# Kernel tuning notes

Hardware: AMD Instinct MI355X
Metric: run time of the kernel (lower is better)

## Reference

```python
import jax, jax.numpy as jnp
import numpy as np

NOT_EPSILON = 1.0
B, Q, K, T = 2, 512, 512, 256  # batch, num queries, num keys, dims


def swishmax(x, axis):
    # x * exp(x - max) / (sum(|x * exp(x - max)|) + 1)
    xexp = x * jnp.exp(x - jnp.max(x, axis=axis, keepdims=True))
    return xexp / (jnp.sum(jnp.abs(xexp), axis=axis, keepdims=True) + NOT_EPSILON)


def setup_inputs() -> dict:
    key = jax.random.key(0)
    ks = jax.random.split(key, 8)
    s = 1.0 / np.sqrt(T)
    return {
        "query_tokens": jax.random.normal(ks[0], (B, Q, T), jnp.float32),
        "key_tokens": jax.random.normal(ks[1], (B, K, T), jnp.float32),
        "value_tokens": jax.random.normal(ks[2], (B, K, T), jnp.float32),
        "Wk": jax.random.normal(ks[3], (T, T), jnp.float32) * s,
        "Wq": jax.random.normal(ks[4], (T, T), jnp.float32) * s,
        "Wva": jax.random.normal(ks[5], (T, T), jnp.float32) * s,
        "Wal": jax.random.normal(ks[6], (T, T), jnp.float32) * s,
        "Wvo": jax.random.normal(ks[7], (T, T), jnp.float32) * s,
    }


def reference(query_tokens, key_tokens, value_tokens, Wk, Wq, Wva, Wal, Wvo):
    # torch nn.Linear: y = x @ W.T (no biases)
    k = jnp.einsum('bkt,ut->bku', key_tokens, Wk)      # [B,K,T]
    q = jnp.einsum('bqt,ut->bqu', query_tokens, Wq)    # [B,Q,T]
    # elementwise outer product over token pairs: [B,K,Q,T]
    raw = k[:, :, None, :] * q[:, None, :, :]
    logits = jnp.einsum('bkqt,ut->bkqu', raw, Wal)     # [B,K,Q,T]
    scale = swishmax(logits, axis=-2)                  # normalize over Q
    v = jnp.einsum('bkt,ut->bku', value_tokens, Wva)   # [B,K,T]
    values_scaled = v[:, :, None, :] * scale           # [B,K,Q,T]
    value_sum = values_scaled.sum(axis=-3)             # sum over K -> [B,Q,T]
    return jnp.einsum('bqt,ut->bqu', value_sum, Wvo)   # [B,Q,T]
```

## Files before the change

### kernel.cpp

```cpp
#include <hip/hip_runtime.h>
#include <cstdint>


typedef short bf16x8 __attribute__((ext_vector_type(8)));
typedef float f32x4  __attribute__((ext_vector_type(4)));

__device__ inline float bf2f(short s) {
  return __uint_as_float(((unsigned)(unsigned short)s) << 16);
}
__device__ inline unsigned packrn(float lo, float hi) {
  return __builtin_amdgcn_perm(__float_as_uint(hi) + 0x8000u,
                               __float_as_uint(lo) + 0x8000u, 0x07060302u);
}

#define FMA16()                                                                 \
  c[0][0] += a.x*w.x; c[0][1] += a.x*w.y; c[0][2] += a.x*w.z; c[0][3] += a.x*w.w; \
  c[1][0] += a.y*w.x; c[1][1] += a.y*w.y; c[1][2] += a.y*w.z; c[1][3] += a.y*w.w; \
  c[2][0] += a.z*w.x; c[2][1] += a.z*w.y; c[2][2] += a.z*w.z; c[2][3] += a.z*w.w; \
  c[3][0] += a.w*w.x; c[3][1] += a.w*w.y; c[3][2] += a.w*w.z; c[3][3] += a.w*w.w;

#define GEMM_BODY(X, WT)                                                        \
  __shared__ __align__(16) float As[16][68];                                    \
  __shared__ __align__(16) float Ws[16][64];                                    \
  const int tid = threadIdx.x;                                                  \
  const int tx4 = (tid & 15) * 4;                                               \
  const int ty4 = (tid >> 4) * 4;                                               \
  const int m0 = blockIdx.x * 64, u0 = blockIdx.y * 64;                         \
  const int lmi = tid >> 2, lc4 = (tid & 3) * 4;                                \
  const int lr  = tid >> 4, lu4 = (tid & 15) * 4;                               \
  float c[4][4] = {};                                                           \
  _Pragma("unroll 1")                                                           \
  for (int t0 = 0; t0 < 256; t0 += 16) {                                        \
    const float4 xa = *(const float4*)&(X)[(size_t)(m0 + lmi) * 256 + t0 + lc4];\
    const float4 wb = *(const float4*)&(WT)[(size_t)(t0 + lr) * 256 + u0 + lu4];\
    __syncthreads();                                                            \
    As[lc4 + 0][lmi] = xa.x; As[lc4 + 1][lmi] = xa.y;                           \
    As[lc4 + 2][lmi] = xa.z; As[lc4 + 3][lmi] = xa.w;                           \
    *(float4*)&Ws[lr][lu4] = wb;                                                \
    __syncthreads();                                                            \
    _Pragma("unroll")                                                           \
    for (int t = 0; t < 16; ++t) {                                              \
      const float4 a = *(const float4*)&As[t][ty4];                             \
      const float4 w = *(const float4*)&Ws[t][tx4];                             \
      FMA16();                                                                  \
    }                                                                           \
  }

__global__ __launch_bounds__(256) void prep(
    const float* __restrict__ Wk, const float* __restrict__ Wq,
    const float* __restrict__ Wva, const float* __restrict__ Wvo,
    const float* __restrict__ Wal, float* __restrict__ WT,
    short* __restrict__ WalF)
{
  const int r = blockIdx.x;
  const int m = blockIdx.y;
  const int t = threadIdx.x;
  if (m < 4) {
    const float* W = (m == 0) ? Wk : (m == 1) ? Wq : (m == 2) ? Wva : Wvo;
    WT[(size_t)m * 65536 + (size_t)t * 256 + r] = W[r * 256 + t];
  } else {
    const float v = Wal[r * 256 + t];
    const int uc = r >> 5, uu = r & 31, cc = t >> 3, j = t & 7;
    WalF[((size_t)(uc * 32 + cc) * 32 + uu) * 8 + j] = (short)packrn(v, v);
  }
}

__global__ __launch_bounds__(256) void proj3(
    const float* __restrict__ key, const float* __restrict__ value,
    const float* __restrict__ query, const float* __restrict__ WT,
    float* __restrict__ kproj, float* __restrict__ vproj, short* __restrict__ qpF)
{
  const int z = blockIdx.z;
  const float* X  = (z == 0) ? key : (z == 1) ? value : query;
  const float* Wt = WT + (size_t)((z == 0) ? 0 : (z == 1) ? 2 : 1) * 65536;
  GEMM_BODY(X, Wt);
  if (z == 2) {
    const int tbase = u0 + tx4;
    const int ks = tbase >> 5, l4f = (tbase & 31) >> 3, j0 = tbase & 7;
#pragma unroll
    for (int i = 0; i < 4; ++i) {
      const int m = m0 + ty4 + i;
      const int bb = m >> 9, q = m & 511;
      const int g = q >> 4, l15q = q & 15;
      const size_t idx = ((size_t)(((bb * 32 + g) * 8 + ks) * 64) + l4f * 16 + l15q) * 8 + j0;
      uint2 s; s.x = packrn(c[i][0], c[i][1]); s.y = packrn(c[i][2], c[i][3]);
      *(uint2*)&qpF[idx] = s;
    }
  } else {
    float* C = (z == 0) ? kproj : vproj;
#pragma unroll
    for (int i = 0; i < 4; ++i)
      *(float4*)&C[(size_t)(m0 + ty4 + i) * 256 + u0 + tx4] =
          make_float4(c[i][0], c[i][1], c[i][2], c[i][3]);
  }
}

__global__ __launch_bounds__(256) void gemm_out(
    const float* __restrict__ X, const float* __restrict__ WT, float* __restrict__ out)
{
  GEMM_BODY(X, WT);
#pragma unroll
  for (int i = 0; i < 4; ++i)
    *(float4*)&out[(size_t)(m0 + ty4 + i) * 256 + u0 + tx4] =
        make_float4(c[i][0], c[i][1], c[i][2], c[i][3]);
}

__global__ __launch_bounds__(1024, 4) void kernelC(
    const short* __restrict__ qpF, const float* __restrict__ kproj,
    const float* __restrict__ vproj, const short* __restrict__ WalF,
    float* __restrict__ vsum)
{
  __shared__ __align__(16) short W2F[8192];
  __shared__ float mS[16][32];
  __shared__ float sS[16][32];
  __shared__ float gS[32];

  const int kt = blockIdx.x, uc = blockIdx.y, b = blockIdx.z;
  const int u0 = uc * 32, k0 = kt * 32;
  const int tid = threadIdx.x;
  const int lane = tid & 63, w = tid >> 6;
  const int l15 = lane & 15, l4 = lane >> 4;
  const int c8 = tid >> 5;

  float wvf[8];
  {
    const bf16x8 wv = *(const bf16x8*)&WalF[((size_t)uc * 1024 + tid) * 8];
#pragma unroll
    for (int j = 0; j < 8; ++j) wvf[j] = bf2f(wv[j]);
  }

  const short* qbase = qpF + (size_t)b * 131072;
  const f32x4 z4 = {0.f, 0.f, 0.f, 0.f};
  f32x4 acc[2][2] = {z4, z4, z4, z4};

#pragma unroll 1
  for (int kk = 0; kk < 32; ++kk) {
    const int k = k0 + kk;
    const long krow = (long)(b * 512 + k) * 256;
    const f32x4 kp0 = *(const f32x4*)&kproj[krow + c8 * 8];
    const f32x4 kp1 = *(const f32x4*)&kproj[krow + c8 * 8 + 4];
    __syncthreads();
    {
      uint4 st;
      st.x = packrn(wvf[0] * kp0[0], wvf[1] * kp0[1]);
      st.y = packrn(wvf[2] * kp0[2], wvf[3] * kp0[3]);
      st.z = packrn(wvf[4] * kp1[0], wvf[5] * kp1[1]);
      st.w = packrn(wvf[6] * kp1[2], wvf[7] * kp1[3]);
      *(uint4*)&W2F[tid * 8] = st;
    }
    __syncthreads();

    f32x4 lg[2][2] = {z4, z4, z4, z4};
#pragma unroll
    for (int ks = 0; ks < 8; ++ks) {
      const bf16x8 qa0 = *(const bf16x8*)&qbase[(((w * 2 + 0) * 8 + ks) * 64 + lane) * 8];
      const bf16x8 qa1 = *(const bf16x8*)&qbase[(((w * 2 + 1) * 8 + ks) * 64 + lane) * 8];
      const bf16x8 wf0 = *(const bf16x8*)&W2F[(((ks * 4 + l4) * 32) + l15) * 8];
      const bf16x8 wf1 = *(const bf16x8*)&W2F[(((ks * 4 + l4) * 32) + 16 + l15) * 8];
      lg[0][0] = __builtin_amdgcn_mfma_f32_16x16x32_bf16(qa0, wf0, lg[0][0], 0, 0, 0);
      lg[1][0] = __builtin_amdgcn_mfma_f32_16x16x32_bf16(qa1, wf0, lg[1][0], 0, 0, 0);
      lg[0][1] = __builtin_amdgcn_mfma_f32_16x16x32_bf16(qa0, wf1, lg[0][1], 0, 0, 0);
      lg[1][1] = __builtin_amdgcn_mfma_f32_16x16x32_bf16(qa1, wf1, lg[1][1], 0, 0, 0);
    }

#pragma unroll
    for (int ug = 0; ug < 2; ++ug) {
      float m = lg[0][ug][0];
#pragma unroll
      for (int qg = 0; qg < 2; ++qg)
#pragma unroll
        for (int i = 0; i < 4; ++i) m = fmaxf(m, lg[qg][ug][i]);
      float s = 0.f;
#pragma unroll
      for (int qg = 0; qg < 2; ++qg)
#pragma unroll
        for (int i = 0; i < 4; ++i) {
          const float x = lg[qg][ug][i];
          const float p = x * __expf(x);
          lg[qg][ug][i] = p;
          s += fabsf(p);
        }
      m = fmaxf(m, __shfl_xor(m, 16));
      m = fmaxf(m, __shfl_xor(m, 32));
      s += __shfl_xor(s, 16);
      s += __shfl_xor(s, 32);
      if (l4 == 0) { mS[w][ug * 16 + l15] = m; sS[w][ug * 16 + l15] = s; }
    }
    __syncthreads();
    if (tid < 32) {
      float M = mS[0][tid], S = sS[0][tid];
#pragma unroll
      for (int r = 1; r < 16; ++r) { M = fmaxf(M, mS[r][tid]); S += sS[r][tid]; }
      const float em = __expf(-M);
      gS[tid] = vproj[krow + u0 + tid] * em / fmaf(S, em, 1.0f);
    }
    __syncthreads();
    const float g0 = gS[l15], g1 = gS[16 + l15];
#pragma unroll
    for (int qg = 0; qg < 2; ++qg)
#pragma unroll
      for (int i = 0; i < 4; ++i) {
        acc[qg][0][i] = fmaf(g0, lg[qg][0][i], acc[qg][0][i]);
        acc[qg][1][i] = fmaf(g1, lg[qg][1][i], acc[qg][1][i]);
      }
  }

#pragma unroll
  for (int qg = 0; qg < 2; ++qg)
#pragma unroll
    for (int ug = 0; ug < 2; ++ug)
#pragma unroll
      for (int i = 0; i < 4; ++i)
        atomicAdd(&vsum[(size_t)(b * 512 + w * 32 + qg * 16 + l4 * 4 + i) * 256 +
                        u0 + ug * 16 + l15],
                  acc[qg][ug][i]);
}

extern "C" void kernel_launch(void* const* d_in, const int* in_sizes, int n_in,
                              void* d_out, int out_size, void* d_ws, size_t ws_size,
                              hipStream_t stream) {
  const float* query = (const float*)d_in[0];
  const float* key   = (const float*)d_in[1];
  const float* value = (const float*)d_in[2];
  const float* Wk    = (const float*)d_in[3];
  const float* Wq    = (const float*)d_in[4];
  const float* Wva   = (const float*)d_in[5];
  const float* Wal   = (const float*)d_in[6];
  const float* Wvo   = (const float*)d_in[7];
  float* ws = (float*)d_ws;

  float* WT    = ws;
  float* kproj = ws + 262144;
  float* vproj = kproj + 262144;
  float* vsum  = vproj + 262144;
  short* qpF   = (short*)(vsum + 262144);
  short* WalF  = qpF + 262144;
  float* out   = (float*)d_out;

  hipMemsetAsync(vsum, 0, 262144 * sizeof(float), stream);

  prep<<<dim3(256, 5), 256, 0, stream>>>(Wk, Wq, Wva, Wvo, Wal, WT, WalF);
  proj3<<<dim3(16, 4, 3), 256, 0, stream>>>(key, value, query, WT, kproj, vproj, qpF);
  kernelC<<<dim3(16, 8, 2), 1024, 0, stream>>>(qpF, kproj, vproj, WalF, vsum);
  gemm_out<<<dim3(16, 4), 256, 0, stream>>>(vsum, WT + 3 * 65536, out);
}
```

Measured before the change: 211.6 us.

## Drop prep kernel and memset, register-cache query fragments, double-buffer W2F in kernelC

The transpose and prep kernel and the memset are removed. The GEMMs now read row-major weights directly, and the Wal reformat plus the vsum zeroing run as an extra z-slice of proj3, cutting the launch count from five to three. kernelC moves to 512 threads, with each wave keeping its 64 query rows of bf16 fragments resident in registers instead of reloading them every k. The per-k W2F tile is double-buffered, with the next k's kproj loaded ahead so one barrier per iteration is removed. Shared-memory atomics with a rotating triple buffer replace the two-stage max/sum reduction. This adds heavy register pressure (128 VGPRs of query fragments plus accumulators), which may hurt occupancy.

```diff
diff --git a/kernel.cpp b/kernel.cpp
--- a/kernel.cpp
+++ b/kernel.cpp
@@ -11,6 +11,14 @@
 __device__ inline unsigned packrn(float lo, float hi) {
   return __builtin_amdgcn_perm(__float_as_uint(hi) + 0x8000u,
                                __float_as_uint(lo) + 0x8000u, 0x07060302u);
+}
+__device__ inline unsigned encM(float f) {
+  unsigned k = (unsigned)__float_as_int(f);
+  return (k & 0x80000000u) ? ~k : (k | 0x80000000u);
+}
+__device__ inline float decM(unsigned k) {
+  int i = (k & 0x80000000u) ? (int)(k ^ 0x80000000u) : (int)~k;
+  return __int_as_float(i);
 }
 
 #define FMA16()                                                                 \
@@ -19,24 +27,24 @@
   c[2][0] += a.z*w.x; c[2][1] += a.z*w.y; c[2][2] += a.z*w.z; c[2][3] += a.z*w.w; \
   c[3][0] += a.w*w.x; c[3][1] += a.w*w.y; c[3][2] += a.w*w.z; c[3][3] += a.w*w.w;
 
-#define GEMM_BODY(X, WT)                                                        \
+#define GEMM_BODY_RM(X, W)                                                      \
   __shared__ __align__(16) float As[16][68];                                    \
-  __shared__ __align__(16) float Ws[16][64];                                    \
+  __shared__ __align__(16) float Ws[16][68];                                    \
   const int tid = threadIdx.x;                                                  \
   const int tx4 = (tid & 15) * 4;                                               \
   const int ty4 = (tid >> 4) * 4;                                               \
   const int m0 = blockIdx.x * 64, u0 = blockIdx.y * 64;                         \
   const int lmi = tid >> 2, lc4 = (tid & 3) * 4;                                \
-  const int lr  = tid >> 4, lu4 = (tid & 15) * 4;                               \
   float c[4][4] = {};                                                           \
   _Pragma("unroll 1")                                                           \
   for (int t0 = 0; t0 < 256; t0 += 16) {                                        \
     const float4 xa = *(const float4*)&(X)[(size_t)(m0 + lmi) * 256 + t0 + lc4];\
-    const float4 wb = *(const float4*)&(WT)[(size_t)(t0 + lr) * 256 + u0 + lu4];\
+    const float4 wb = *(const float4*)&(W)[(size_t)(u0 + lmi) * 256 + t0 + lc4];\
     __syncthreads();                                                            \
     As[lc4 + 0][lmi] = xa.x; As[lc4 + 1][lmi] = xa.y;                           \
     As[lc4 + 2][lmi] = xa.z; As[lc4 + 3][lmi] = xa.w;                           \
-    *(float4*)&Ws[lr][lu4] = wb;                                                \
+    Ws[lc4 + 0][lmi] = wb.x; Ws[lc4 + 1][lmi] = wb.y;                           \
+    Ws[lc4 + 2][lmi] = wb.z; Ws[lc4 + 3][lmi] = wb.w;                           \
     __syncthreads();                                                            \
     _Pragma("unroll")                                                           \
     for (int t = 0; t < 16; ++t) {                                              \
@@ -46,34 +54,34 @@
     }                                                                           \
   }
 
-__global__ __launch_bounds__(256) void prep(
-    const float* __restrict__ Wk, const float* __restrict__ Wq,
-    const float* __restrict__ Wva, const float* __restrict__ Wvo,
-    const float* __restrict__ Wal, float* __restrict__ WT,
-    short* __restrict__ WalF)
-{
-  const int r = blockIdx.x;
-  const int m = blockIdx.y;
-  const int t = threadIdx.x;
-  if (m < 4) {
-    const float* W = (m == 0) ? Wk : (m == 1) ? Wq : (m == 2) ? Wva : Wvo;
-    WT[(size_t)m * 65536 + (size_t)t * 256 + r] = W[r * 256 + t];
-  } else {
-    const float v = Wal[r * 256 + t];
-    const int uc = r >> 5, uu = r & 31, cc = t >> 3, j = t & 7;
-    WalF[((size_t)(uc * 32 + cc) * 32 + uu) * 8 + j] = (short)packrn(v, v);
-  }
-}
-
 __global__ __launch_bounds__(256) void proj3(
     const float* __restrict__ key, const float* __restrict__ value,
-    const float* __restrict__ query, const float* __restrict__ WT,
-    float* __restrict__ kproj, float* __restrict__ vproj, short* __restrict__ qpF)
+    const float* __restrict__ query, const float* __restrict__ Wk,
+    const float* __restrict__ Wq, const float* __restrict__ Wva,
+    const float* __restrict__ Wal, float* __restrict__ kproj,
+    float* __restrict__ vproj, short* __restrict__ qpF,
+    short* __restrict__ WalF, float* __restrict__ vsum)
 {
   const int z = blockIdx.z;
-  const float* X  = (z == 0) ? key : (z == 1) ? value : query;
-  const float* Wt = WT + (size_t)((z == 0) ? 0 : (z == 1) ? 2 : 1) * 65536;
-  GEMM_BODY(X, Wt);
+  if (z == 3) {
+    const int p = blockIdx.x * 4 + blockIdx.y;
+    const int t256 = threadIdx.x;
+#pragma unroll
+    for (int e = 0; e < 4; ++e) {
+      const int d = p * 1024 + t256 * 4 + e;
+      const int j = d & 7, uu = (d >> 3) & 31, c8g = d >> 8;
+      const int ucx = c8g >> 5, cc = c8g & 31;
+      const float v = Wal[(ucx * 32 + uu) * 256 + cc * 8 + j];
+      WalF[d] = (short)packrn(v, v);
+    }
+    float4* vz = (float4*)(vsum + p * 4096);
+#pragma unroll
+    for (int e = 0; e < 4; ++e) vz[t256 * 4 + e] = make_float4(0.f, 0.f, 0.f, 0.f);
+    return;
+  }
+  const float* X = (z == 0) ? key : (z == 1) ? value : query;
+  const float* W = (z == 0) ? Wk  : (z == 1) ? Wva   : Wq;
+  GEMM_BODY_RM(X, W);
   if (z == 2) {
     const int tbase = u0 + tx4;
     const int ks = tbase >> 5, l4f = (tbase & 31) >> 3, j0 = tbase & 7;
@@ -96,83 +104,133 @@
 }
 
 __global__ __launch_bounds__(256) void gemm_out(
-    const float* __restrict__ X, const float* __restrict__ WT, float* __restrict__ out)
+    const float* __restrict__ X, const float* __restrict__ W, float* __restrict__ out)
 {
-  GEMM_BODY(X, WT);
+  GEMM_BODY_RM(X, W);
 #pragma unroll
   for (int i = 0; i < 4; ++i)
     *(float4*)&out[(size_t)(m0 + ty4 + i) * 256 + u0 + tx4] =
         make_float4(c[i][0], c[i][1], c[i][2], c[i][3]);
 }
 
-__global__ __launch_bounds__(1024, 4) void kernelC(
+union Frag { bf16x8 v; unsigned u[4]; };
+
+__global__ __launch_bounds__(512, 2) void kernelC(
     const short* __restrict__ qpF, const float* __restrict__ kproj,
     const float* __restrict__ vproj, const short* __restrict__ WalF,
     float* __restrict__ vsum)
 {
-  __shared__ __align__(16) short W2F[8192];
-  __shared__ float mS[16][32];
-  __shared__ float sS[16][32];
-  __shared__ float gS[32];
+  __shared__ __align__(16) short W2F[2][8192];
+  __shared__ float vpS[32 * 33];
+  __shared__ unsigned statM[96];
+  __shared__ float statS[96];
 
   const int kt = blockIdx.x, uc = blockIdx.y, b = blockIdx.z;
   const int u0 = uc * 32, k0 = kt * 32;
   const int tid = threadIdx.x;
   const int lane = tid & 63, w = tid >> 6;
   const int l15 = lane & 15, l4 = lane >> 4;
-  const int c8 = tid >> 5;
-
-  float wvf[8];
+  const int uu = tid & 31, c8 = tid >> 5;
+
+  if (tid < 96) { statM[tid] = 0u; statS[tid] = 0.f; }
   {
-    const bf16x8 wv = *(const bf16x8*)&WalF[((size_t)uc * 1024 + tid) * 8];
-#pragma unroll
-    for (int j = 0; j < 8; ++j) wvf[j] = bf2f(wv[j]);
+    const int kk = tid >> 4, uu2 = (tid & 15) * 2;
+    const float2 v2 = *(const float2*)&vproj[(size_t)(b * 512 + k0 + kk) * 256 + u0 + uu2];
+    vpS[kk * 33 + uu2] = v2.x; vpS[kk * 33 + uu2 + 1] = v2.y;
+  }
+
+  float wl0[8], wl1[8];
+  {
+    const bf16x8 w0 = *(const bf16x8*)&WalF[((size_t)(uc * 32 + c8) * 32 + uu) * 8];
+    const bf16x8 w1 = *(const bf16x8*)&WalF[((size_t)(uc * 32 + c8 + 16) * 32 + uu) * 8];
+#pragma unroll
+    for (int j = 0; j < 8; ++j) { wl0[j] = bf2f(w0[j]); wl1[j] = bf2f(w1[j]); }
   }
 
   const short* qbase = qpF + (size_t)b * 131072;
+  Frag qa[4][8];
+#pragma unroll
+  for (int qg = 0; qg < 4; ++qg)
+#pragma unroll
+    for (int ks = 0; ks < 8; ++ks) {
+      qa[qg][ks].v = *(const bf16x8*)&qbase[(((size_t)(w * 4 + qg) * 8 + ks) * 64 + lane) * 8];
+      asm volatile("" : "+v"(qa[qg][ks].u[0]), "+v"(qa[qg][ks].u[1]),
+                        "+v"(qa[qg][ks].u[2]), "+v"(qa[qg][ks].u[3]));
+    }
+
+  {
+    const long krow = (long)(b * 512 + k0) * 256;
+    const f32x4 a0 = *(const f32x4*)&kproj[krow + c8 * 8];
+    const f32x4 a1 = *(const f32x4*)&kproj[krow + c8 * 8 + 4];
+    const f32x4 b0 = *(const f32x4*)&kproj[krow + (c8 + 16) * 8];
+    const f32x4 b1 = *(const f32x4*)&kproj[krow + (c8 + 16) * 8 + 4];
+    uint4 st;
+    st.x = packrn(wl0[0] * a0[0], wl0[1] * a0[1]);
+    st.y = packrn(wl0[2] * a0[2], wl0[3] * a0[3]);
+    st.z = packrn(wl0[4] * a1[0], wl0[5] * a1[1]);
+    st.w = packrn(wl0[6] * a1[2], wl0[7] * a1[3]);
+    *(uint4*)&W2F[0][(c8 * 32 + uu) * 8] = st;
+    st.x = packrn(wl1[0] * b0[0], wl1[1] * b0[1]);
+    st.y = packrn(wl1[2] * b0[2], wl1[3] * b0[3]);
+    st.z = packrn(wl1[4] * b1[0], wl1[5] * b1[1]);
+    st.w = packrn(wl1[6] * b1[2], wl1[7] * b1[3]);
+    *(uint4*)&W2F[0][((c8 + 16) * 32 + uu) * 8] = st;
+  }
+  __syncthreads();
+
   const f32x4 z4 = {0.f, 0.f, 0.f, 0.f};
-  f32x4 acc[2][2] = {z4, z4, z4, z4};
+  f32x4 acc[4][2] = {z4, z4, z4, z4, z4, z4, z4, z4};
 
 #pragma unroll 1
   for (int kk = 0; kk < 32; ++kk) {
-    const int k = k0 + kk;
-    const long krow = (long)(b * 512 + k) * 256;
-    const f32x4 kp0 = *(const f32x4*)&kproj[krow + c8 * 8];
-    const f32x4 kp1 = *(const f32x4*)&kproj[krow + c8 * 8 + 4];
-    __syncthreads();
-    {
+    const int cs = kk & 1, ss = kk % 3;
+
+    f32x4 a0, a1, b0, b1;
+    if (kk < 31) {
+      const long krn = (long)(b * 512 + k0 + kk + 1) * 256;
+      a0 = *(const f32x4*)&kproj[krn + c8 * 8];
+      a1 = *(const f32x4*)&kproj[krn + c8 * 8 + 4];
+      b0 = *(const f32x4*)&kproj[krn + (c8 + 16) * 8];
+      b1 = *(const f32x4*)&kproj[krn + (c8 + 16) * 8 + 4];
+    }
+
+    f32x4 lg[4][2] = {z4, z4, z4, z4, z4, z4, z4, z4};
+#pragma unroll
+    for (int ks = 0; ks < 8; ++ks) {
+      const bf16x8 f0 = *(const bf16x8*)&W2F[cs][((ks * 4 + l4) * 32 + l15) * 8];
+      const bf16x8 f1 = *(const bf16x8*)&W2F[cs][((ks * 4 + l4) * 32 + 16 + l15) * 8];
+#pragma unroll
+      for (int qg = 0; qg < 4; ++qg) {
+        lg[qg][0] = __builtin_amdgcn_mfma_f32_16x16x32_bf16(qa[qg][ks].v, f0, lg[qg][0], 0, 0, 0);
+        lg[qg][1] = __builtin_amdgcn_mfma_f32_16x16x32_bf16(qa[qg][ks].v, f1, lg[qg][1], 0, 0, 0);
+      }
+    }
+
+    if (kk < 31) {
       uint4 st;
-      st.x = packrn(wvf[0] * kp0[0], wvf[1] * kp0[1]);
-      st.y = packrn(wvf[2] * kp0[2], wvf[3] * kp0[3]);
-      st.z = packrn(wvf[4] * kp1[0], wvf[5] * kp1[1]);
-      st.w = packrn(wvf[6] * kp1[2], wvf[7] * kp1[3]);
-      *(uint4*)&W2F[tid * 8] = st;
-    }
-    __syncthreads();
-
-    f32x4 lg[2][2] = {z4, z4, z4, z4};
-#pragma unroll
-    for (int ks = 0; ks < 8; ++ks) {
-      const bf16x8 qa0 = *(const bf16x8*)&qbase[(((w * 2 + 0) * 8 + ks) * 64 + lane) * 8];
-      const bf16x8 qa1 = *(const bf16x8*)&qbase[(((w * 2 + 1) * 8 + ks) * 64 + lane) * 8];
-      const bf16x8 wf0 = *(const bf16x8*)&W2F[(((ks * 4 + l4) * 32) + l15) * 8];
-      const bf16x8 wf1 = *(const bf16x8*)&W2F[(((ks * 4 + l4) * 32) + 16 + l15) * 8];
-      lg[0][0] = __builtin_amdgcn_mfma_f32_16x16x32_bf16(qa0, wf0, lg[0][0], 0, 0, 0);
-      lg[1][0] = __builtin_amdgcn_mfma_f32_16x16x32_bf16(qa1, wf0, lg[1][0], 0, 0, 0);
-      lg[0][1] = __builtin_amdgcn_mfma_f32_16x16x32_bf16(qa0, wf1, lg[0][1], 0, 0, 0);
-      lg[1][1] = __builtin_amdgcn_mfma_f32_16x16x32_bf16(qa1, wf1, lg[1][1], 0, 0, 0);
-    }
-
+      st.x = packrn(wl0[0] * a0[0], wl0[1] * a0[1]);
+      st.y = packrn(wl0[2] * a0[2], wl0[3] * a0[3]);
+      st.z = packrn(wl0[4] * a1[0], wl0[5] * a1[1]);
+      st.w = packrn(wl0[6] * a1[2], wl0[7] * a1[3]);
+      *(uint4*)&W2F[cs ^ 1][(c8 * 32 + uu) * 8] = st;
+      st.x = packrn(wl1[0] * b0[0], wl1[1] * b0[1]);
+      st.y = packrn(wl1[2] * b0[2], wl1[3] * b0[3]);
+      st.z = packrn(wl1[4] * b1[0], wl1[5] * b1[1]);
+      st.w = packrn(wl1[6] * b1[2], wl1[7] * b1[3]);
+      *(uint4*)&W2F[cs ^ 1][((c8 + 16) * 32 + uu) * 8] = st;
+    }
+
+    float Mv[2], Sv[2];
 #pragma unroll
     for (int ug = 0; ug < 2; ++ug) {
       float m = lg[0][ug][0];
 #pragma unroll
-      for (int qg = 0; qg < 2; ++qg)
+      for (int qg = 0; qg < 4; ++qg)
 #pragma unroll
         for (int i = 0; i < 4; ++i) m = fmaxf(m, lg[qg][ug][i]);
       float s = 0.f;
 #pragma unroll
-      for (int qg = 0; qg < 2; ++qg)
+      for (int qg = 0; qg < 4; ++qg)
 #pragma unroll
         for (int i = 0; i < 4; ++i) {
           const float x = lg[qg][ug][i];
@@ -184,34 +242,40 @@
       m = fmaxf(m, __shfl_xor(m, 32));
       s += __shfl_xor(s, 16);
       s += __shfl_xor(s, 32);
-      if (l4 == 0) { mS[w][ug * 16 + l15] = m; sS[w][ug * 16 + l15] = s; }
+      Mv[ug] = m; Sv[ug] = s;
+    }
+    if (l4 == 0) {
+      atomicMax(&statM[ss * 32 + l15],      encM(Mv[0]));
+      atomicMax(&statM[ss * 32 + 16 + l15], encM(Mv[1]));
+      atomicAdd(&statS[ss * 32 + l15],      Sv[0]);
+      atomicAdd(&statS[ss * 32 + 16 + l15], Sv[1]);
     }
     __syncthreads();
-    if (tid < 32) {
-      float M = mS[0][tid], S = sS[0][tid];
-#pragma unroll
-      for (int r = 1; r < 16; ++r) { M = fmaxf(M, mS[r][tid]); S += sS[r][tid]; }
+
+#pragma unroll
+    for (int ug = 0; ug < 2; ++ug) {
+      const int ui = ug * 16 + l15;
+      const float M = decM(statM[ss * 32 + ui]);
+      const float S = statS[ss * 32 + ui];
       const float em = __expf(-M);
-      gS[tid] = vproj[krow + u0 + tid] * em / fmaf(S, em, 1.0f);
-    }
-    __syncthreads();
-    const float g0 = gS[l15], g1 = gS[16 + l15];
-#pragma unroll
-    for (int qg = 0; qg < 2; ++qg)
-#pragma unroll
-      for (int i = 0; i < 4; ++i) {
-        acc[qg][0][i] = fmaf(g0, lg[qg][0][i], acc[qg][0][i]);
-        acc[qg][1][i] = fmaf(g1, lg[qg][1][i], acc[qg][1][i]);
-      }
-  }
-
-#pragma unroll
-  for (int qg = 0; qg < 2; ++qg)
+      const float g = vpS[kk * 33 + ui] * em / fmaf(S, em, 1.0f);
+#pragma unroll
+      for (int qg = 0; qg < 4; ++qg)
+#pragma unroll
+        for (int i = 0; i < 4; ++i)
+          acc[qg][ug][i] = fmaf(g, lg[qg][ug][i], acc[qg][ug][i]);
+    }
+    const int rs = (kk + 2) % 3;
+    if (tid < 32) { statM[rs * 32 + tid] = 0u; statS[rs * 32 + tid] = 0.f; }
+  }
+
+#pragma unroll
+  for (int qg = 0; qg < 4; ++qg)
 #pragma unroll
     for (int ug = 0; ug < 2; ++ug)
 #pragma unroll
       for (int i = 0; i < 4; ++i)
-        atomicAdd(&vsum[(size_t)(b * 512 + w * 32 + qg * 16 + l4 * 4 + i) * 256 +
+        atomicAdd(&vsum[(size_t)(b * 512 + w * 64 + qg * 16 + l4 * 4 + i) * 256 +
                         u0 + ug * 16 + l15],
                   acc[qg][ug][i]);
 }
@@ -229,18 +293,15 @@
   const float* Wvo   = (const float*)d_in[7];
   float* ws = (float*)d_ws;
 
-  float* WT    = ws;
-  float* kproj = ws + 262144;
+  float* kproj = ws;
   float* vproj = kproj + 262144;
   float* vsum  = vproj + 262144;
   short* qpF   = (short*)(vsum + 262144);
   short* WalF  = qpF + 262144;
   float* out   = (float*)d_out;
 
-  hipMemsetAsync(vsum, 0, 262144 * sizeof(float), stream);
-
-  prep<<<dim3(256, 5), 256, 0, stream>>>(Wk, Wq, Wva, Wvo, Wal, WT, WalF);
-  proj3<<<dim3(16, 4, 3), 256, 0, stream>>>(key, value, query, WT, kproj, vproj, qpF);
-  kernelC<<<dim3(16, 8, 2), 1024, 0, stream>>>(qpF, kproj, vproj, WalF, vsum);
-  gemm_out<<<dim3(16, 4), 256, 0, stream>>>(vsum, WT + 3 * 65536, out);
-}
+  proj3<<<dim3(16, 4, 4), 256, 0, stream>>>(key, value, query, Wk, Wq, Wva, Wal,
+                                            kproj, vproj, qpF, WalF, vsum);
+  kernelC<<<dim3(16, 8, 2), 512, 0, stream>>>(qpF, kproj, vproj, WalF, vsum);
+  gemm_out<<<dim3(16, 4), 256, 0, stream>>>(vsum, Wvo, out);
+}
```

Result: faster. 197.8 us (-6.5%).
